# Optimization experiments

Measured on AMD Instinct MI355X. Metric: run time of the kernel, lower is better.

## Reference

```python
import jax, jax.numpy as jnp
import numpy as np

BIT_SIZE = 8
ES_SIZE = 1
IN_F = 2048
OUT_F = 2048
N = 8192


def posit_quantize(x, nbits, es):
    """Round-to-nearest posit(nbits, es) quantization, returned as float32.

    Posit value: sign * useed^k * 2^e * (1+f), useed = 2^(2^es).
    Regime length rlen = k+2 (k>=0) or -k+1 (k<0); fraction bits =
    nbits - 1(sign) - rlen - es, clamped at 0. Magnitudes are clamped to
    [minpos, maxpos] (posits never round a nonzero value to zero/inf).
    """
    two_es = 2 ** es                      # useed = 2**two_es
    npat = nbits - 2
    maxpos = jnp.float32(2.0 ** (two_es * npat))
    minpos = jnp.float32(2.0 ** (-two_es * npat))

    sign = jnp.sign(x)
    ax = jnp.clip(jnp.abs(x), minpos, maxpos)

    s = jnp.floor(jnp.log2(ax))           # integer power-of-two scale
    k = jnp.floor(s / two_es)             # regime value
    rlen = jnp.where(k >= 0, k + 2.0, -k + 1.0)
    fbits = jnp.maximum(nbits - 1.0 - rlen - es, 0.0)

    m = ax * jnp.exp2(-s)                 # mantissa in [1, 2)
    fscale = jnp.exp2(fbits)
    mq = jnp.round(m * fscale) / fscale   # round fraction to fbits
    # carry: mantissa rounded up to 2.0 -> bump exponent
    s = jnp.where(mq >= 2.0, s + 1.0, s)
    mq = jnp.where(mq >= 2.0, 1.0, mq)

    y = sign * mq * jnp.exp2(s)
    y = jnp.clip(y, -maxpos, maxpos)
    return jnp.where(x == 0, jnp.float32(0.0), y).astype(x.dtype)


def setup_inputs() -> dict:
    key = jax.random.key(0)
    kx, kw, kb = jax.random.split(key, 3)
    x = jax.random.normal(kx, (N, IN_F), dtype=jnp.float32)
    bound = 1.0 / np.sqrt(IN_F)  # nn.Linear default init range
    weight = jax.random.uniform(kw, (OUT_F, IN_F), dtype=jnp.float32,
                                minval=-bound, maxval=bound)
    bias = jax.random.uniform(kb, (OUT_F,), dtype=jnp.float32,
                              minval=-bound, maxval=bound)
    return {"x": x, "weight": weight, "bias": bias}


def reference(x, weight, bias):
    xq = posit_quantize(x, BIT_SIZE, ES_SIZE)
    wq = posit_quantize(weight, BIT_SIZE, ES_SIZE)
    bq = posit_quantize(bias, BIT_SIZE, ES_SIZE)
    # y = xq @ wq^T + bq  (nn.Linear)
    return jnp.einsum('ni,oi->no', xq, wq) + bq
```

## Files before the change

### kernel.cpp

```cpp
#include <hip/hip_runtime.h>

typedef __attribute__((ext_vector_type(8))) short bf16x8;
typedef __attribute__((ext_vector_type(4))) float f32x4;

__device__ __forceinline__ float posit_q(float x) {
  float ax = fabsf(x);
  ax = fmaxf(ax, 0x1p-12f);
  ax = fminf(ax, 0x1p12f);
  int s = (int)(__float_as_uint(ax) >> 23) - 127;
  int k = s >> 1;
  int rlen = (k >= 0) ? (k + 2) : (1 - k);
  int fbits = 6 - rlen;
  fbits = fbits < 0 ? 0 : fbits;
  float m = ax * __uint_as_float((unsigned)(127 - s) << 23);
  float fs = (float)(1 << fbits);
  float inv_fs = __uint_as_float((unsigned)(127 - fbits) << 23);
  float mq = rintf(m * fs) * inv_fs;
  if (mq >= 2.0f) { s += 1; mq = 1.0f; }
  float y = mq * __uint_as_float((unsigned)(127 + s) << 23);
  y = fminf(y, 0x1p12f);
  y = copysignf(y, x);
  return (x == 0.0f) ? 0.0f : y;
}

__device__ __forceinline__ ushort4 quant4_bf16(float4 v) {
  ushort4 o;
  o.x = (ushort)(__float_as_uint(posit_q(v.x)) >> 16);
  o.y = (ushort)(__float_as_uint(posit_q(v.y)) >> 16);
  o.z = (ushort)(__float_as_uint(posit_q(v.z)) >> 16);
  o.w = (ushort)(__float_as_uint(posit_q(v.w)) >> 16);
  return o;
}

__global__ void posit_quant_all(const float* __restrict__ x,
                                const float* __restrict__ w,
                                const float* __restrict__ b,
                                ushort* __restrict__ Xq,
                                ushort* __restrict__ Wq,
                                float* __restrict__ bq,
                                int nx4, int nw4, int nb4) {
  int i = blockIdx.x * blockDim.x + threadIdx.x;
  if (i < nx4) {
    ((ushort4*)Xq)[i] = quant4_bf16(((const float4*)x)[i]);
  } else if (i < nx4 + nw4) {
    int j = i - nx4;
    ((ushort4*)Wq)[j] = quant4_bf16(((const float4*)w)[j]);
  } else if (i < nx4 + nw4 + nb4) {
    int j = i - nx4 - nw4;
    float4 v = ((const float4*)b)[j];
    float4 o;
    o.x = posit_q(v.x); o.y = posit_q(v.y);
    o.z = posit_q(v.z); o.w = posit_q(v.w);
    ((float4*)bq)[j] = o;
  }
}

__device__ __forceinline__ void gl_lds16(const ushort* g, ushort* l) {
  __builtin_amdgcn_global_load_lds(
      (const __attribute__((address_space(1))) void*)g,
      (__attribute__((address_space(3))) void*)l,
      16, 0, 0);
}

#define BAR() do { __builtin_amdgcn_s_barrier(); \
                   __builtin_amdgcn_sched_barrier(0); } while (0)

__global__ __launch_bounds__(512, 2) void posit_gemm(
    const ushort* __restrict__ A, const ushort* __restrict__ B,
    const float* __restrict__ bq, float* __restrict__ C,
    int M, int N, int K) {
  __shared__ ushort lds[65536];

  const int tid = threadIdx.x;
  const int wave = tid >> 6;
  const int lane = tid & 63;
  const int wm = wave >> 2;
  const int wn = wave & 3;
  const int m0 = blockIdx.y << 8;
  const int n0 = blockIdx.x << 8;

  const int srow = (wave << 4) + (lane >> 2);
  const int sk = (((lane & 3) ^ (lane >> 4)) << 3);
  const ushort* Ag = A + (size_t)(m0 + srow) * K + sk;
  const ushort* Bg = B + (size_t)(n0 + srow) * K + sk;
  const size_t rstep = (size_t)128 * K;
  const int sbase = wave << 9;

#define STAGE(Lb, kt) do {                                         \
    const ushort* _ag = Ag + ((size_t)(kt) << 5);                  \
    const ushort* _bg = Bg + ((size_t)(kt) << 5);                  \
    gl_lds16(_ag,         (Lb) + sbase);                           \
    gl_lds16(_ag + rstep, (Lb) + 4096 + sbase);                    \
    gl_lds16(_bg,         (Lb) + 8192 + sbase);                    \
    gl_lds16(_bg + rstep, (Lb) + 12288 + sbase);                   \
  } while (0)

  const int fr = lane & 15;
  const int t4 = lane >> 4;
  const int sl = ((t4 ^ (fr >> 2)) << 3);
  const int arl = (((wm << 7) + fr) << 5) + sl;
  const int brl = (((wn << 6) + fr) << 5) + sl + 8192;

  f32x4 acc[8][4];
#pragma unroll
  for (int i = 0; i < 8; i++)
#pragma unroll
    for (int j = 0; j < 4; j++) acc[i][j] = (f32x4){0.f, 0.f, 0.f, 0.f};

#define COMP(Lb) do {                                              \
    bf16x8 fa[8], fb[4];                                           \
    _Pragma("unroll")                                              \
    for (int i = 0; i < 8; i++)                                    \
      fa[i] = *(const bf16x8*)((Lb) + arl + (i << 9));             \
    _Pragma("unroll")                                              \
    for (int j = 0; j < 4; j++)                                    \
      fb[j] = *(const bf16x8*)((Lb) + brl + (j << 9));             \
    _Pragma("unroll")                                              \
    for (int i = 0; i < 8; i++)                                    \
      _Pragma("unroll")                                            \
      for (int j = 0; j < 4; j++)                                  \
        acc[i][j] = __builtin_amdgcn_mfma_f32_16x16x32_bf16(       \
            fa[i], fb[j], acc[i][j], 0, 0, 0);                     \
  } while (0)

  const int T = K >> 5;

  STAGE(lds, 0);
  STAGE(lds + 16384, 1);
  asm volatile("s_waitcnt vmcnt(4)" ::: "memory");
  BAR();

#pragma unroll 1
  for (int it = 0; it < (T >> 2); ++it) {
    const int t0 = it << 2;
#pragma unroll
    for (int u = 0; u < 4; ++u) {
      const int t = t0 + u;
      ushort* const cb = lds + (u << 14);
      ushort* const nb = lds + (((u + 2) & 3) << 14);
      if (t + 2 < T) {
        STAGE(nb, t + 2);
        asm volatile("s_waitcnt vmcnt(4)" ::: "memory");
      } else {
        asm volatile("s_waitcnt vmcnt(0)" ::: "memory");
      }
      BAR();
      COMP(cb);
    }
  }

  const int row0 = m0 + (wm << 7) + (t4 << 2);
  const int col0 = n0 + (wn << 6) + fr;
#pragma unroll
  for (int j = 0; j < 4; j++) {
    const int col = col0 + (j << 4);
    const float bv = bq[col];
#pragma unroll
    for (int i = 0; i < 8; i++) {
      const int row = row0 + (i << 4);
#pragma unroll
      for (int r = 0; r < 4; r++)
        C[(size_t)(row + r) * N + col] = acc[i][j][r] + bv;
    }
  }
}

extern "C" void kernel_launch(void* const* d_in, const int* in_sizes, int n_in,
                              void* d_out, int out_size, void* d_ws, size_t ws_size,
                              hipStream_t stream) {
  const float* x = (const float*)d_in[0];
  const float* w = (const float*)d_in[1];
  const float* bias = (const float*)d_in[2];
  float* out = (float*)d_out;

  const int out_f = in_sizes[2];
  const int in_f = in_sizes[1] / out_f;
  const int m = in_sizes[0] / in_f;
  const int k = in_f;

  ushort* Xq = (ushort*)d_ws;
  ushort* Wq = Xq + (size_t)m * k;
  float* bquant = (float*)(Wq + (size_t)out_f * k);

  const int nx4 = in_sizes[0] / 4;
  const int nw4 = in_sizes[1] / 4;
  const int nb4 = in_sizes[2] / 4;
  const int total4 = nx4 + nw4 + nb4;
  posit_quant_all<<<(total4 + 255) / 256, 256, 0, stream>>>(
      x, w, bias, Xq, Wq, bquant, nx4, nw4, nb4);

  dim3 grid(out_f / 256, m / 256);
  posit_gemm<<<grid, 512, 0, stream>>>(Xq, Wq, bquant, out, m, out_f, k);
}
```

Baseline: 189.0 us.

## Deepen GEMM LDS pipeline to five buffers with prefetch distance three

Grows the shared-memory ring from four to five 32 KB stages and prefetches three K-tiles ahead instead of two, with dynamic buffer indices replacing the unrolled four-way loop. It also changes the XOR swizzle used for both the global-to-LDS store and the fragment read, aiming to reduce LDS bank conflicts. The goal is to hide more global-load latency. The cost is 160 KB of LDS per block, which likely allows only one 512-thread block per CU instead of two. The runtime-indexed buffers also add some address arithmetic.

```diff
diff --git a/kernel.cpp b/kernel.cpp
--- a/kernel.cpp
+++ b/kernel.cpp
@@ -69,7 +69,7 @@
     const ushort* __restrict__ A, const ushort* __restrict__ B,
     const float* __restrict__ bq, float* __restrict__ C,
     int M, int N, int K) {
-  __shared__ ushort lds[65536];
+  __shared__ ushort lds[81920];
 
   const int tid = threadIdx.x;
   const int wave = tid >> 6;
@@ -80,7 +80,7 @@
   const int n0 = blockIdx.x << 8;
 
   const int srow = (wave << 4) + (lane >> 2);
-  const int sk = (((lane & 3) ^ (lane >> 4)) << 3);
+  const int sk = (((lane & 3) ^ ((lane >> 3) & 3)) << 3);
   const ushort* Ag = A + (size_t)(m0 + srow) * K + sk;
   const ushort* Bg = B + (size_t)(n0 + srow) * K + sk;
   const size_t rstep = (size_t)128 * K;
@@ -97,7 +97,7 @@
 
   const int fr = lane & 15;
   const int t4 = lane >> 4;
-  const int sl = ((t4 ^ (fr >> 2)) << 3);
+  const int sl = ((t4 ^ ((fr >> 1) & 3)) << 3);
   const int arl = (((wm << 7) + fr) << 5) + sl;
   const int brl = (((wn << 6) + fr) << 5) + sl + 8192;
 
@@ -125,28 +125,33 @@
 
   const int T = K >> 5;
 
-  STAGE(lds, 0);
+  STAGE(lds,         0);
   STAGE(lds + 16384, 1);
-  asm volatile("s_waitcnt vmcnt(4)" ::: "memory");
+  STAGE(lds + 32768, 2);
+  asm volatile("s_waitcnt vmcnt(8)" ::: "memory");
   BAR();
 
+  int cbi = 0;
+  int sbi = 3;
 #pragma unroll 1
-  for (int it = 0; it < (T >> 2); ++it) {
-    const int t0 = it << 2;
-#pragma unroll
-    for (int u = 0; u < 4; ++u) {
-      const int t = t0 + u;
-      ushort* const cb = lds + (u << 14);
-      ushort* const nb = lds + (((u + 2) & 3) << 14);
-      if (t + 2 < T) {
-        STAGE(nb, t + 2);
-        asm volatile("s_waitcnt vmcnt(4)" ::: "memory");
-      } else {
-        asm volatile("s_waitcnt vmcnt(0)" ::: "memory");
-      }
-      BAR();
-      COMP(cb);
-    }
+  for (int t = 0; t < T - 3; ++t) {
+    ushort* const cb = lds + (cbi << 14);
+    ushort* const sb = lds + (sbi << 14);
+    STAGE(sb, t + 3);
+    asm volatile("s_waitcnt vmcnt(8)" ::: "memory");
+    BAR();
+    COMP(cb);
+    cbi = (cbi == 4) ? 0 : cbi + 1;
+    sbi = (sbi == 4) ? 0 : sbi + 1;
+  }
+#pragma unroll 1
+  for (int t = T - 3; t < T; ++t) {
+    ushort* const cb = lds + (cbi << 14);
+    if (t == T - 3)      asm volatile("s_waitcnt vmcnt(4)" ::: "memory");
+    else if (t == T - 2) asm volatile("s_waitcnt vmcnt(0)" ::: "memory");
+    BAR();
+    COMP(cb);
+    cbi = (cbi == 4) ? 0 : cbi + 1;
   }
 
   const int row0 = m0 + (wm << 7) + (t4 << 2);
```

New measurement: 186.5 us. About the same (-1.4%).
